# Optimization experiments

Measured on AMD Instinct MI355X. Metric: run time of the kernel, lower is better.

The kernel has to match this reference:

```python
import jax, jax.numpy as jnp
import numpy as np

N_LAYERS = 6
D_MODEL = 272          # num_variables
D_STATE = 64           # d_state
D_INNER = 2 * D_MODEL  # expand=2 -> 544
D_CONV = 4
DT_RANK = 17           # ceil(272/16)
N_SCORES = 4
B, L = 4, 2048


def setup_inputs():
    key = jax.random.key(0)
    ks = jax.random.split(key, 10)
    def rn(k, shape, s=0.02):
        return jax.random.normal(k, shape, dtype=jnp.float32) * s
    A_init = jnp.broadcast_to(jnp.arange(1, D_STATE + 1, dtype=jnp.float32), (N_LAYERS, D_INNER, D_STATE))
    return {
        "x": jax.random.normal(ks[0], (B, L, D_MODEL), dtype=jnp.float32),
        "ln_w": jnp.ones((N_LAYERS, D_MODEL), jnp.float32),
        "ln_b": jnp.zeros((N_LAYERS, D_MODEL), jnp.float32),
        "in_proj_w": rn(ks[1], (N_LAYERS, 2 * D_INNER, D_MODEL)),
        "conv_w": rn(ks[2], (N_LAYERS, D_INNER, D_CONV), 0.2),
        "conv_b": jnp.zeros((N_LAYERS, D_INNER), jnp.float32),
        "x_proj_w": rn(ks[3], (N_LAYERS, DT_RANK + 2 * D_STATE, D_INNER)),
        "dt_proj_w": rn(ks[4], (N_LAYERS, D_INNER, DT_RANK), 0.1),
        "dt_proj_b": rn(ks[5], (N_LAYERS, D_INNER), 0.5),
        "A_log": jnp.log(A_init),
        "Dskip": jnp.ones((N_LAYERS, D_INNER), jnp.float32),
        "out_proj_w": rn(ks[6], (N_LAYERS, D_MODEL, D_INNER)),
        "reg_w": rn(ks[7], (N_SCORES, D_MODEL)),
        "reg_b": jnp.zeros((N_SCORES,), jnp.float32),
    }


def _layernorm(x, w, b, eps=1e-5):
    mu = x.mean(-1, keepdims=True)
    var = ((x - mu) ** 2).mean(-1, keepdims=True)
    return (x - mu) * jax.lax.rsqrt(var + eps) * w + b


def _selective_scan(u, delta, A, Bm, C, Dd):
    # u, delta: (b,l,d); Bm, C: (b,l,n); A: (d,n); Dd: (d,)
    def step(h, inp):
        d_t, B_t, C_t, u_t = inp                           # (b,d),(b,n),(b,n),(b,d)
        dA = jnp.exp(d_t[:, :, None] * A)                  # (b,d,n)
        h = dA * h + (d_t * u_t)[:, :, None] * B_t[:, None, :]
        return h, jnp.einsum('bdn,bn->bd', h, C_t)
    h0 = jnp.zeros((u.shape[0], A.shape[0], A.shape[1]), u.dtype)
    xs = tuple(jnp.swapaxes(a, 0, 1) for a in (delta, Bm, C, u))  # time-major
    _, ys = jax.lax.scan(step, h0, xs)
    return jnp.swapaxes(ys, 0, 1) + u * Dd


def _mamba_block(x, ln_w, ln_b, Wi, cw, cb, Wx, Wdt, bdt, A_log, Dd, Wo):
    h = _layernorm(x, ln_w, ln_b)
    xi, z = jnp.split(h @ Wi.T, 2, axis=-1)                # (b,l,d_inner) each
    xp = jnp.pad(xi, ((0, 0), (D_CONV - 1, 0), (0, 0)))    # causal depthwise conv
    xc = sum(xp[:, k:k + xi.shape[1], :] * cw[:, k] for k in range(D_CONV)) + cb
    xc = jax.nn.silu(xc)
    dbl = xc @ Wx.T                                        # (b,l,dt_rank+2n)
    dt, Bm, C = jnp.split(dbl, [DT_RANK, DT_RANK + D_STATE], axis=-1)
    delta = jax.nn.softplus(dt @ Wdt.T + bdt)
    y = _selective_scan(xc, delta, -jnp.exp(A_log), Bm, C, Dd)
    y = y * jax.nn.silu(z)
    return x + y @ Wo.T                                    # residual


def reference(x, ln_w, ln_b, in_proj_w, conv_w, conv_b, x_proj_w, dt_proj_w, dt_proj_b, A_log, Dskip, out_proj_w, reg_w, reg_b):
    for i in range(N_LAYERS):
        x = _mamba_block(x, ln_w[i], ln_b[i], in_proj_w[i], conv_w[i], conv_b[i],
                         x_proj_w[i], dt_proj_w[i], dt_proj_b[i], A_log[i], Dskip[i], out_proj_w[i])
    feat = x.mean(axis=1)                                  # (b, d_model)
    scores = feat @ reg_w.T + reg_b                        # (b, n_scores)
    return (scores, feat)
```

## Files before the change

### kernel.cpp

```cpp
#include <hip/hip_runtime.h>
#include <hip/hip_bf16.h>
#include <math.h>

#define NL 6
#define DM 272
#define DS 64
#define DI 544
#define DTR 17
#define NSC 4
#define BB 4
#define LL 2048
#define MTOK (BB*LL)
#define TCH 128
#define CH  16
#define DQ  (DI/4)

typedef __attribute__((ext_vector_type(8))) short bf16x8;
typedef __attribute__((ext_vector_type(4))) float f32x4;

__device__ __forceinline__ float sigmoidf_(float x){ return 1.0f/(1.0f+__expf(-x)); }
__device__ __forceinline__ unsigned short f2bfu(float x){
    union { __hip_bfloat16 h; unsigned short u; } c; c.h = __float2bfloat16(x); return c.u;
}
__device__ __forceinline__ float bfu2f(unsigned short u){ return __uint_as_float(((unsigned)u)<<16); }
__device__ __forceinline__ float exp2x(float x){ float r; asm("v_exp_f32 %0, %1" : "=v"(r) : "v"(x)); return r; }

#define DPPADD(x, ctrl) x += __int_as_float(__builtin_amdgcn_update_dpp(0, __float_as_int(x), ctrl, 0xf, 0xf, true))
__device__ __forceinline__ float wsum64(float x){
    DPPADD(x, 0x111); DPPADD(x, 0x112); DPPADD(x, 0x114); DPPADD(x, 0x118);
    DPPADD(x, 0x142); DPPADD(x, 0x143);
    return x;
}

__global__ __launch_bounds__(256) void ln_kernel(const float* __restrict__ X,
                          const float* __restrict__ w,
                          const float* __restrict__ b,
                          unsigned short* __restrict__ Hb)
{
    int wave = threadIdx.x >> 6;
    int lane = threadIdx.x & 63;
    int tok = blockIdx.x*4 + wave;
    const float* xr = X + (size_t)tok*DM;
    float v[5];
    float s=0.f, ss=0.f;
    #pragma unroll
    for (int j=0;j<5;++j){
        int idx = lane + j*64;
        float x = (idx < DM) ? xr[idx] : 0.f;
        v[j]=x; s+=x; ss+=x*x;
    }
    #pragma unroll
    for (int off=1; off<64; off<<=1){ s += __shfl_xor(s,off); ss += __shfl_xor(ss,off); }
    float mu  = s * (1.0f/DM);
    float var = ss*(1.0f/DM) - mu*mu;
    float inv = 1.0f/sqrtf(var + 1e-5f);
    unsigned short* hr = Hb + (size_t)tok*DM;
    #pragma unroll
    for (int j=0;j<5;++j){
        int idx = lane + j*64;
        if (idx<DM) hr[idx] = f2bfu((v[j]-mu)*inv*w[idx] + b[idx]);
    }
}

template<bool RESID, bool OUTBF16>
__global__ __launch_bounds__(256) void gmfma(const unsigned short* __restrict__ A, int lda,
                     const unsigned short* __restrict__ W, int ldw,
                     void* __restrict__ Cv, int ldc,
                     const float* __restrict__ R, int ldr,
                     int N, int K)
{
    __shared__ unsigned short As[128*40];
    __shared__ unsigned short Bs[128*40];
    int bm = blockIdx.x*128, bn = blockIdx.y*128;
    int tid = threadIdx.x;
    int lane = tid & 63, wave = tid >> 6;
    int wm = wave >> 1, wn = wave & 1;
    f32x4 acc[4][4] = {};
    int r16 = lane & 15, kg = (lane >> 4) * 8;
    for (int k0=0; k0<K; k0+=32){
        #pragma unroll
        for (int it=0; it<2; ++it){
            int cid = tid + it*256;
            int row = cid >> 2, kq = (cid & 3)*8;
            int kk = k0 + kq;
            uint4 za = make_uint4(0,0,0,0);
            if (kk < K) za = *(const uint4*)(A + (size_t)(bm+row)*lda + kk);
            *(uint4*)&As[row*40 + kq] = za;
            uint4 zb = make_uint4(0,0,0,0);
            int wr = bn + row;
            if (wr < N && kk < K) zb = *(const uint4*)(W + (size_t)wr*ldw + kk);
            *(uint4*)&Bs[row*40 + kq] = zb;
        }
        __syncthreads();
        bf16x8 af[4], bfr[4];
        #pragma unroll
        for (int mi=0; mi<4; ++mi)
            af[mi] = *(bf16x8*)&As[(wm*64 + mi*16 + r16)*40 + kg];
        #pragma unroll
        for (int ni=0; ni<4; ++ni)
            bfr[ni] = *(bf16x8*)&Bs[(wn*64 + ni*16 + r16)*40 + kg];
        #pragma unroll
        for (int mi=0; mi<4; ++mi)
            #pragma unroll
            for (int ni=0; ni<4; ++ni)
                acc[mi][ni] = __builtin_amdgcn_mfma_f32_16x16x32_bf16(af[mi], bfr[ni], acc[mi][ni], 0, 0, 0);
        __syncthreads();
    }
    int rowt = (lane >> 4)*4, colt = lane & 15;
    #pragma unroll
    for (int mi=0; mi<4; ++mi){
        #pragma unroll
        for (int ni=0; ni<4; ++ni){
            int col = bn + wn*64 + ni*16 + colt;
            if (col < N){
                #pragma unroll
                for (int j=0; j<4; ++j){
                    int row = bm + wm*64 + mi*16 + rowt + j;
                    float v = acc[mi][ni][j];
                    if (RESID) v += R[(size_t)row*ldr + col];
                    if (OUTBF16)
                        ((unsigned short*)Cv)[(size_t)row*ldc + col] = f2bfu(v);
                    else
                        ((float*)Cv)[(size_t)row*ldc + col] = v;
                }
            }
        }
    }
}

__global__ __launch_bounds__(256) void conv_t2_kernel(const unsigned short* __restrict__ XZb,
                                 const float* __restrict__ cw,
                                 const float* __restrict__ cb,
                                 unsigned short* __restrict__ XCtb,
                                 unsigned short* __restrict__ Gtb,
                                 unsigned short* __restrict__ XCb)
{
    __shared__ float xi[67][69];
    __shared__ float zz[64][69];
    int bid = blockIdx.x;
    int b  = bid >> 8;
    int rem = bid & 255;
    int t0 = (rem >> 3)*64;
    int d0 = (rem & 7)*68;
    int tid = threadIdx.x;
    for (int li = tid; li < 67*17; li += 256){
        int row = li / 17, q = li - row*17;
        int tg = t0 - 3 + row;
        float4 v = make_float4(0.f,0.f,0.f,0.f);
        if (tg >= 0){
            ushort4 u4 = *(const ushort4*)(XZb + ((size_t)b*LL + tg)*(2*DI) + d0 + q*4);
            v.x = bfu2f(u4.x); v.y = bfu2f(u4.y); v.z = bfu2f(u4.z); v.w = bfu2f(u4.w);
        }
        xi[row][q*4+0]=v.x; xi[row][q*4+1]=v.y; xi[row][q*4+2]=v.z; xi[row][q*4+3]=v.w;
    }
    for (int li = tid; li < 64*17; li += 256){
        int row = li / 17, q = li - row*17;
        ushort4 u4 = *(const ushort4*)(XZb + ((size_t)b*LL + t0 + row)*(2*DI) + DI + d0 + q*4);
        zz[row][q*4+0]=bfu2f(u4.x); zz[row][q*4+1]=bfu2f(u4.y);
        zz[row][q*4+2]=bfu2f(u4.z); zz[row][q*4+3]=bfu2f(u4.w);
    }
    __syncthreads();
    int t = tid & 63;
    int dw = tid >> 6;
    float xcreg[17];
    #pragma unroll
    for (int i=0; i<17; ++i){
        int dl = dw + i*4;
        int d = d0 + dl;
        const float* cwd = cw + d*4;
        float acc = cb[d];
        #pragma unroll
        for (int k=0;k<4;++k) acc = fmaf(xi[t+k][dl], cwd[k], acc);
        float xc = acc * sigmoidf_(acc);
        float z  = zz[t][dl];
        size_t o = ((size_t)b*DI + d)*LL + t0 + t;
        XCtb[o] = f2bfu(xc);
        Gtb[o]  = f2bfu(z * sigmoidf_(z));
        xcreg[i] = xc;
    }
    __syncthreads();
    #pragma unroll
    for (int i=0; i<17; ++i) zz[t][dw + i*4] = xcreg[i];
    __syncthreads();
    for (int li = tid; li < 64*17; li += 256){
        int row = li / 17, q = li - row*17;
        ushort4 v;
        v.x = f2bfu(zz[row][q*4+0]); v.y = f2bfu(zz[row][q*4+1]);
        v.z = f2bfu(zz[row][q*4+2]); v.w = f2bfu(zz[row][q*4+3]);
        *(ushort4*)&XCb[((size_t)b*LL + t0 + row)*DI + d0 + q*4] = v;
    }
}

__global__ __launch_bounds__(256) void dt_t2_kernel(const float* __restrict__ DBLb,
                          const float* __restrict__ Wdt,
                          const float* __restrict__ bdt,
                          float* __restrict__ DELt)
{
    __shared__ float dtv[64*19];
    __shared__ float wl[68*17];
    int bid = blockIdx.x;
    int b  = bid >> 8;
    int rem = bid & 255;
    int t0 = (rem >> 3)*64;
    int d0 = (rem & 7)*68;
    int tid = threadIdx.x;
    for (int li = tid; li < 64*17; li += 256){
        int row = li / 17, col = li - row*17;
        dtv[row*19 + col] = DBLb[((size_t)b*LL + t0 + row)*145 + col];
    }
    for (int li = tid; li < 68*17; li += 256)
        wl[li] = Wdt[(size_t)d0*17 + li];
    __syncthreads();
    int t = tid & 63;
    #pragma unroll 1
    for (int dl = tid >> 6; dl < 68; dl += 4){
        float s = bdt[d0 + dl];
        #pragma unroll
        for (int r=0;r<DTR;++r) s = fmaf(dtv[t*19 + r], wl[dl*17 + r], s);
        float sp = (s > 20.f) ? s : log1pf(__expf(s));
        DELt[((size_t)b*DI + d0 + dl)*LL + t0 + t] = sp;
    }
}

__global__ __launch_bounds__(256) void scan_a(const float* __restrict__ DELt,
                       const unsigned short* __restrict__ XCtb,
                       const float* __restrict__ DBLb,
                       const float* __restrict__ A_log,
                       float* __restrict__ Q,
                       float* __restrict__ S)
{
    __shared__ float2 dlb[4][4][64];
    __shared__ float Bsh[64][68];
    int tid = threadIdx.x;
    int wave = tid >> 6, lane = tid & 63;
    float2 (*Db)[64] = dlb[wave];
    int wid = blockIdx.x*4 + wave;
    int dd = wid % DQ;
    int c  = (wid / DQ) % CH;
    int b  = wid / (DQ*CH);
    int d0 = dd, d1 = dd+DQ, d2 = dd+2*DQ, d3 = dd+3*DQ;
    const float L2E = 1.44269504f;
    float Av0 = -__expf(A_log[d0*DS + lane]) * L2E;
    float Av1 = -__expf(A_log[d1*DS + lane]) * L2E;
    float Av2 = -__expf(A_log[d2*DS + lane]) * L2E;
    float Av3 = -__expf(A_log[d3*DS + lane]) * L2E;
    float h0=0.f,h1=0.f,h2=0.f,h3=0.f, ds0=0.f,ds1=0.f,ds2=0.f,ds3=0.f;
    size_t rb0 = ((size_t)b*DI + d0)*LL + c*TCH;
    size_t rb1 = ((size_t)b*DI + d1)*LL + c*TCH;
    size_t rb2 = ((size_t)b*DI + d2)*LL + c*TCH;
    size_t rb3 = ((size_t)b*DI + d3)*LL + c*TCH;
    const float* pBB = DBLb + ((size_t)b*LL + (size_t)c*TCH)*145;
    float rg[16];
    #pragma unroll
    for (int k=0;k<16;++k){
        int li = tid + k*256;
        rg[k] = pBB[(size_t)(li>>6)*145 + 17 + (li&63)];
    }
    for (int blk=0; blk<TCH/64; ++blk){
        __syncthreads();
        #pragma unroll
        for (int k=0;k<16;++k){
            int li = tid + k*256;
            Bsh[li>>6][li&63] = rg[k];
        }
        __syncthreads();
        if (blk+1 < TCH/64){
            const float* nb = pBB + (size_t)(blk+1)*64*145;
            #pragma unroll
            for (int k=0;k<16;++k){
                int li = tid + k*256;
                rg[k] = nb[(size_t)(li>>6)*145 + 17 + (li&63)];
            }
        }
        size_t o0 = rb0 + blk*64 + lane, o1 = rb1 + blk*64 + lane;
        size_t o2 = rb2 + blk*64 + lane, o3 = rb3 + blk*64 + lane;
        float dl0 = DELt[o0], dl1 = DELt[o1], dl2 = DELt[o2], dl3 = DELt[o3];
        float du0 = dl0*bfu2f(XCtb[o0]), du1 = dl1*bfu2f(XCtb[o1]);
        float du2 = dl2*bfu2f(XCtb[o2]), du3 = dl3*bfu2f(XCtb[o3]);
        ds0 += dl0; ds1 += dl1; ds2 += dl2; ds3 += dl3;
        Db[0][lane] = make_float2(dl0, du0);
        Db[1][lane] = make_float2(dl1, du1);
        Db[2][lane] = make_float2(dl2, du2);
        Db[3][lane] = make_float2(dl3, du3);
        #pragma unroll 1
        for (int g=0; g<8; ++g){
            const float2* q0 = &Db[0][g*8];
            const float2* q1 = &Db[1][g*8];
            const float2* q2 = &Db[2][g*8];
            const float2* q3 = &Db[3][g*8];
            #pragma unroll
            for (int i=0; i<8; ++i){
                float Bv = Bsh[g*8+i][lane];
                float2 a0=q0[i], a1=q1[i], a2=q2[i], a3=q3[i];
                h0 = fmaf(exp2x(a0.x*Av0), h0, a0.y*Bv);
                h1 = fmaf(exp2x(a1.x*Av1), h1, a1.y*Bv);
                h2 = fmaf(exp2x(a2.x*Av2), h2, a2.y*Bv);
                h3 = fmaf(exp2x(a3.x*Av3), h3, a3.y*Bv);
            }
        }
    }
    size_t q0i = ((size_t)b*DI + d0)*CH + c, q1i = ((size_t)b*DI + d1)*CH + c;
    size_t q2i = ((size_t)b*DI + d2)*CH + c, q3i = ((size_t)b*DI + d3)*CH + c;
    Q[q0i*64 + lane] = h0; Q[q1i*64 + lane] = h1;
    Q[q2i*64 + lane] = h2; Q[q3i*64 + lane] = h3;
    float s0 = wsum64(ds0), s1 = wsum64(ds1), s2 = wsum64(ds2), s3 = wsum64(ds3);
    if (lane == 63){ S[q0i]=s0; S[q1i]=s1; S[q2i]=s2; S[q3i]=s3; }
}

__global__ __launch_bounds__(256) void scan_c(const float* __restrict__ DELt,
                       const unsigned short* __restrict__ XCtb,
                       const unsigned short* __restrict__ Gtb,
                       const float* __restrict__ DBLb,
                       const float* __restrict__ A_log,
                       const float* __restrict__ Dskip,
                       const float* __restrict__ Q,
                       const float* __restrict__ S,
                       unsigned short* __restrict__ Yb)
{
    __shared__ float P[4][2][4][76];
    __shared__ float Ypark[4][2][4];
    __shared__ float2 dlb[4][2][64];
    __shared__ unsigned short Yst[64][12];
    int tid = threadIdx.x;
    int wave = tid >> 6, lane = tid & 63;
    float (*Pr0)[76] = P[wave][0];
    float (*Pr1)[76] = P[wave][1];
    float* Yp0 = Ypark[wave][0];
    float* Yp1 = Ypark[wave][1];
    float2* Db0 = dlb[wave][0];
    float2* Db1 = dlb[wave][1];
    int wid = blockIdx.x*4 + wave;
    int dd = wid % (DI/2);
    int c  = (wid / (DI/2)) % CH;
    int b  = wid / ((DI/2)*CH);
    int d0 = dd, d1 = dd + DI/2;
    int wid0 = blockIdx.x*4;
    int dd0b = wid0 % (DI/2);
    int cB = (wid0 / (DI/2)) % CH;
    int bB = wid0 / ((DI/2)*CH);
    const float L2E = 1.44269504f;
    float Av0 = -__expf(A_log[d0*DS + lane]) * L2E;
    float Av1 = -__expf(A_log[d1*DS + lane]) * L2E;
    float Dd0 = Dskip[d0], Dd1 = Dskip[d1];
    size_t q0 = ((size_t)b*DI + d0)*CH, q1 = ((size_t)b*DI + d1)*CH;
    float h0=0.f, h1=0.f;
    for (int j=0; j<c; ++j){
        h0 = fmaf(exp2x(Av0*S[q0+j]), h0, Q[(q0+j)*64 + lane]);
        h1 = fmaf(exp2x(Av1*S[q1+j]), h1, Q[(q1+j)*64 + lane]);
    }
    size_t rb0 = ((size_t)b*DI + d0)*LL + c*TCH;
    size_t rb1 = ((size_t)b*DI + d1)*LL + c*TCH;
    const float* pB = DBLb + ((size_t)b*LL + c*TCH)*145;
    int fr = lane >> 4, fq = (lane & 15)*4;
    for (int blk=0; blk<TCH/64; ++blk){
        size_t o0 = rb0 + blk*64 + lane, o1 = rb1 + blk*64 + lane;
        float dl0 = DELt[o0], dl1 = DELt[o1];
        float ul0 = bfu2f(XCtb[o0]), ul1 = bfu2f(XCtb[o1]);
        float gl0 = bfu2f(Gtb[o0]),  gl1 = bfu2f(Gtb[o1]);
        Db0[lane] = make_float2(dl0, dl0*ul0);
        Db1[lane] = make_float2(dl1, dl1*ul1);
        float y0=0.f, y1=0.f;
        const float* p = pB + (size_t)blk*64*145;
        #pragma unroll 1
        for (int f=0; f<16; ++f){
            const float2* db0 = &Db0[f*4];
            const float2* db1 = &Db1[f*4];
            #pragma unroll
            for (int i=0; i<4; ++i){
                float Bv = p[17+lane];
                float Cv = p[81+lane];
                float2 a0 = db0[i], a1 = db1[i];
                h0 = fmaf(exp2x(a0.x*Av0), h0, a0.y*Bv);
                h1 = fmaf(exp2x(a1.x*Av1), h1, a1.y*Bv);
                Pr0[i][lane] = h0*Cv;
                Pr1[i][lane] = h1*Cv;
                p += 145;
            }
            float4 xa0 = *(const float4*)&Pr0[fr][fq];
            float s0 = (xa0.x+xa0.y)+(xa0.z+xa0.w);
            DPPADD(s0,0x111); DPPADD(s0,0x112); DPPADD(s0,0x114); DPPADD(s0,0x118);
            float4 xa1 = *(const float4*)&Pr1[fr][fq];
            float s1 = (xa1.x+xa1.y)+(xa1.z+xa1.w);
            DPPADD(s1,0x111); DPPADD(s1,0x112); DPPADD(s1,0x114); DPPADD(s1,0x118);
            if ((lane & 15) == 15){ Yp0[fr] = s0; Yp1[fr] = s1; }
            float g0 = Yp0[lane & 3];
            float g1 = Yp1[lane & 3];
            if ((lane >> 2) == f){ y0 = g0; y1 = g1; }
        }
        Yst[lane][wave]     = f2bfu((y0 + ul0*Dd0)*gl0);
        Yst[lane][4 + wave] = f2bfu((y1 + ul1*Dd1)*gl1);
        __syncthreads();
        if (tid < 128){
            int row = tid & 63, grp = tid >> 6;
            ushort4 v = *(const ushort4*)&Yst[row][grp*4];
            size_t trow = (size_t)bB*LL + (size_t)cB*TCH + blk*64 + row;
            *(ushort4*)&Yb[trow*DI + dd0b + grp*(DI/2)] = v;
        }
        __syncthreads();
    }
}

__global__ __launch_bounds__(256) void wconv_kernel(const float* __restrict__ src,
                            unsigned short* __restrict__ dst,
                            int total, int kin, int kout)
{
    int idx = blockIdx.x*256 + threadIdx.x;
    if (idx >= total) return;
    int r = idx / kout, c = idx - r*kout;
    float v = (c < kin) ? src[(size_t)r*kin + c] : 0.f;
    dst[idx] = f2bfu(v);
}

__global__ __launch_bounds__(256) void head1_kernel(const float* __restrict__ X,
                             float* __restrict__ Pt)
{
    int b = blockIdx.x >> 6, c = blockIdx.x & 63;
    int tid = threadIdx.x;
    for (int dm = tid; dm < DM; dm += 256){
        float s = 0.f;
        const float* base = X + ((size_t)b*LL + c*32)*DM + dm;
        #pragma unroll 8
        for (int tt=0; tt<32; ++tt) s += base[(size_t)tt*DM];
        Pt[(size_t)(b*64 + c)*DM + dm] = s;
    }
}

__global__ __launch_bounds__(256) void head2_kernel(const float* __restrict__ Pt,
                             const float* __restrict__ reg_w,
                             const float* __restrict__ reg_b,
                             float* __restrict__ out)
{
    __shared__ float feat[DM];
    int b = blockIdx.x, tid = threadIdx.x;
    for (int dm = tid; dm < DM; dm += 256){
        float s = 0.f;
        for (int c=0; c<64; ++c) s += Pt[(size_t)(b*64 + c)*DM + dm];
        float f = s * (1.0f/LL);
        feat[dm] = f;
        out[16 + b*DM + dm] = f;
    }
    __syncthreads();
    if (tid < NSC){
        float s = reg_b[tid];
        const float* wr = reg_w + tid*DM;
        for (int k=0;k<DM;++k) s = fmaf(feat[k], wr[k], s);
        out[b*NSC + tid] = s;
    }
}

extern "C" void kernel_launch(void* const* d_in, const int* in_sizes, int n_in,
                              void* d_out, int out_size, void* d_ws, size_t ws_size,
                              hipStream_t stream)
{
    const float* x_in  = (const float*)d_in[0];
    const float* ln_w  = (const float*)d_in[1];
    const float* ln_b  = (const float*)d_in[2];
    const float* Wi    = (const float*)d_in[3];
    const float* cw    = (const float*)d_in[4];
    const float* cb    = (const float*)d_in[5];
    const float* Wx    = (const float*)d_in[6];
    const float* Wdt   = (const float*)d_in[7];
    const float* bdt   = (const float*)d_in[8];
    const float* A_log = (const float*)d_in[9];
    const float* Dd    = (const float*)d_in[10];
    const float* Wo    = (const float*)d_in[11];
    const float* regw  = (const float*)d_in[12];
    const float* regb  = (const float*)d_in[13];
    float* out = (float*)d_out;

    char* base = (char*)d_ws;
    auto carve = [&](size_t bytes) -> char* {
        char* p = base; base += (bytes + 255) & ~(size_t)255; return p;
    };
    unsigned short* XZb  = (unsigned short*)carve((size_t)MTOK*1088*2);
    unsigned short* XCtb = (unsigned short*)carve((size_t)MTOK*544*2);
    unsigned short* Gtb  = (unsigned short*)carve((size_t)MTOK*544*2);
    float*          DELt = (float*)carve((size_t)MTOK*544*4);
    float*          DBLb = (float*)carve((size_t)MTOK*145*4);
    float*          Xb   = (float*)carve((size_t)MTOK*272*4);
    unsigned short* Yb   = (unsigned short*)carve((size_t)MTOK*544*2);
    char*           SCR  = carve((size_t)MTOK*272*4);
    float*          Sbuf = (float*)carve((size_t)BB*DI*CH*4);
    unsigned short* WiB  = (unsigned short*)carve((size_t)NL*1088*DM*2);
    unsigned short* WxB  = (unsigned short*)carve((size_t)NL*145*DI*2);
    unsigned short* WoB  = (unsigned short*)carve((size_t)NL*272*DI*2);

    unsigned short* Hb  = (unsigned short*)SCR;
    unsigned short* XCb = (unsigned short*)SCR;
    float*          Q   = (float*)SCR;
    float*          Pt  = (float*)SCR;

    (void)hipMemcpyAsync(Xb, x_in, sizeof(float)*(size_t)MTOK*DM, hipMemcpyDeviceToDevice, stream);

    wconv_kernel<<<(NL*1088*DM + 255)/256, 256, 0, stream>>>(Wi, WiB, NL*1088*DM, DM, DM);
    wconv_kernel<<<(NL*145*DI + 255)/256, 256, 0, stream>>>(Wx, WxB, NL*145*DI, DI, DI);
    wconv_kernel<<<(NL*272*DI + 255)/256, 256, 0, stream>>>(Wo, WoB, NL*272*DI, DI, DI);

    for (int l=0; l<NL; ++l){
        ln_kernel<<<MTOK/4, 256, 0, stream>>>(Xb, ln_w + l*DM, ln_b + l*DM, Hb);
        gmfma<false,true><<<dim3(MTOK/128, (2*DI+127)/128), 256, 0, stream>>>(
            Hb, DM, WiB + (size_t)l*2*DI*DM, DM, XZb, 2*DI, nullptr, 0, 2*DI, DM);
        conv_t2_kernel<<<BB*256, 256, 0, stream>>>(XZb, cw + l*DI*4, cb + l*DI, XCtb, Gtb, XCb);
        gmfma<false,false><<<dim3(MTOK/128, 2), 256, 0, stream>>>(
            XCb, DI, WxB + (size_t)l*145*DI, DI, DBLb, 145, nullptr, 0, 145, DI);
        dt_t2_kernel<<<BB*256, 256, 0, stream>>>(DBLb, Wdt + (size_t)l*DI*DTR, bdt + l*DI, DELt);
        scan_a<<<(BB*CH*DQ)/4, 256, 0, stream>>>(DELt, XCtb, DBLb,
                                                 A_log + (size_t)l*DI*DS, Q, Sbuf);
        scan_c<<<(BB*CH*(DI/2))/4, 256, 0, stream>>>(DELt, XCtb, Gtb, DBLb,
                                                     A_log + (size_t)l*DI*DS, Dd + l*DI, Q, Sbuf, Yb);
        gmfma<true,false><<<dim3(MTOK/128, 3), 256, 0, stream>>>(
            Yb, DI, WoB + (size_t)l*DM*DI, DI, Xb, DM, Xb, DM, DM, DI);
    }
    head1_kernel<<<BB*64, 256, 0, stream>>>(Xb, Pt);
    head2_kernel<<<BB, 256, 0, stream>>>(Pt, regw, regb, out);
}
```

Before: 1.587 ms.

## Fuse dt projection and softplus into scan kernels, pack u and gate

Removes the separate dt_t2 kernel and its fp32 delta buffer: both scan passes now recompute delta from the 17 dt-rank values in DBL with a fast exp2/log2 softplus. The conv kernel writes u and the silu gate as one packed 32-bit word instead of two separate bf16 arrays. scan_a also drops its shared-memory staging of B and reads B straight from global memory. This saves one launch and a large amount of global memory traffic, at the cost of doing the dt projection twice and making uncoalesced strided loads of the DBL rows.

```diff
diff --git a/kernel.cpp b/kernel.cpp
--- a/kernel.cpp
+++ b/kernel.cpp
@@ -24,6 +24,11 @@
 }
 __device__ __forceinline__ float bfu2f(unsigned short u){ return __uint_as_float(((unsigned)u)<<16); }
 __device__ __forceinline__ float exp2x(float x){ float r; asm("v_exp_f32 %0, %1" : "=v"(r) : "v"(x)); return r; }
+__device__ __forceinline__ float log2x(float x){ float r; asm("v_log_f32 %0, %1" : "=v"(r) : "v"(x)); return r; }
+__device__ __forceinline__ float softplus_(float s){
+    float sp = 0.6931471806f * log2x(1.0f + exp2x(s * 1.44269504f));
+    return (s > 20.f) ? s : sp;
+}
 
 #define DPPADD(x, ctrl) x += __int_as_float(__builtin_amdgcn_update_dpp(0, __float_as_int(x), ctrl, 0xf, 0xf, true))
 __device__ __forceinline__ float wsum64(float x){
@@ -131,8 +136,7 @@
 __global__ __launch_bounds__(256) void conv_t2_kernel(const unsigned short* __restrict__ XZb,
                                  const float* __restrict__ cw,
                                  const float* __restrict__ cb,
-                                 unsigned short* __restrict__ XCtb,
-                                 unsigned short* __restrict__ Gtb,
+                                 unsigned int* __restrict__ UGt,
                                  unsigned short* __restrict__ XCb)
 {
     __shared__ float xi[67][69];
@@ -174,8 +178,8 @@
         float xc = acc * sigmoidf_(acc);
         float z  = zz[t][dl];
         size_t o = ((size_t)b*DI + d)*LL + t0 + t;
-        XCtb[o] = f2bfu(xc);
-        Gtb[o]  = f2bfu(z * sigmoidf_(z));
+        float g = z * sigmoidf_(z);
+        UGt[o] = (unsigned int)f2bfu(xc) | ((unsigned int)f2bfu(g) << 16);
         xcreg[i] = xc;
     }
     __syncthreads();
@@ -191,46 +195,15 @@
     }
 }
 
-__global__ __launch_bounds__(256) void dt_t2_kernel(const float* __restrict__ DBLb,
-                          const float* __restrict__ Wdt,
-                          const float* __restrict__ bdt,
-                          float* __restrict__ DELt)
-{
-    __shared__ float dtv[64*19];
-    __shared__ float wl[68*17];
-    int bid = blockIdx.x;
-    int b  = bid >> 8;
-    int rem = bid & 255;
-    int t0 = (rem >> 3)*64;
-    int d0 = (rem & 7)*68;
-    int tid = threadIdx.x;
-    for (int li = tid; li < 64*17; li += 256){
-        int row = li / 17, col = li - row*17;
-        dtv[row*19 + col] = DBLb[((size_t)b*LL + t0 + row)*145 + col];
-    }
-    for (int li = tid; li < 68*17; li += 256)
-        wl[li] = Wdt[(size_t)d0*17 + li];
-    __syncthreads();
-    int t = tid & 63;
-    #pragma unroll 1
-    for (int dl = tid >> 6; dl < 68; dl += 4){
-        float s = bdt[d0 + dl];
-        #pragma unroll
-        for (int r=0;r<DTR;++r) s = fmaf(dtv[t*19 + r], wl[dl*17 + r], s);
-        float sp = (s > 20.f) ? s : log1pf(__expf(s));
-        DELt[((size_t)b*DI + d0 + dl)*LL + t0 + t] = sp;
-    }
-}
-
-__global__ __launch_bounds__(256) void scan_a(const float* __restrict__ DELt,
-                       const unsigned short* __restrict__ XCtb,
+__global__ __launch_bounds__(256) void scan_a(const unsigned int* __restrict__ UGt,
                        const float* __restrict__ DBLb,
+                       const float* __restrict__ Wdt,
+                       const float* __restrict__ bdt,
                        const float* __restrict__ A_log,
                        float* __restrict__ Q,
                        float* __restrict__ S)
 {
     __shared__ float2 dlb[4][4][64];
-    __shared__ float Bsh[64][68];
     int tid = threadIdx.x;
     int wave = tid >> 6, lane = tid & 63;
     float2 (*Db)[64] = dlb[wave];
@@ -244,44 +217,40 @@
     float Av1 = -__expf(A_log[d1*DS + lane]) * L2E;
     float Av2 = -__expf(A_log[d2*DS + lane]) * L2E;
     float Av3 = -__expf(A_log[d3*DS + lane]) * L2E;
+    float bd0 = bdt[d0], bd1 = bdt[d1], bd2 = bdt[d2], bd3 = bdt[d3];
     float h0=0.f,h1=0.f,h2=0.f,h3=0.f, ds0=0.f,ds1=0.f,ds2=0.f,ds3=0.f;
     size_t rb0 = ((size_t)b*DI + d0)*LL + c*TCH;
     size_t rb1 = ((size_t)b*DI + d1)*LL + c*TCH;
     size_t rb2 = ((size_t)b*DI + d2)*LL + c*TCH;
     size_t rb3 = ((size_t)b*DI + d3)*LL + c*TCH;
-    const float* pBB = DBLb + ((size_t)b*LL + (size_t)c*TCH)*145;
-    float rg[16];
-    #pragma unroll
-    for (int k=0;k<16;++k){
-        int li = tid + k*256;
-        rg[k] = pBB[(size_t)(li>>6)*145 + 17 + (li&63)];
-    }
+    const float* pB = DBLb + ((size_t)b*LL + (size_t)c*TCH)*145;
     for (int blk=0; blk<TCH/64; ++blk){
-        __syncthreads();
-        #pragma unroll
-        for (int k=0;k<16;++k){
-            int li = tid + k*256;
-            Bsh[li>>6][li&63] = rg[k];
-        }
-        __syncthreads();
-        if (blk+1 < TCH/64){
-            const float* nb = pBB + (size_t)(blk+1)*64*145;
-            #pragma unroll
-            for (int k=0;k<16;++k){
-                int li = tid + k*256;
-                rg[k] = nb[(size_t)(li>>6)*145 + 17 + (li&63)];
-            }
-        }
+        const float* dp = pB + (size_t)(blk*64 + lane)*145;
+        float dv[17];
+        #pragma unroll
+        for (int r=0;r<17;++r) dv[r] = dp[r];
+        float s0=bd0, s1=bd1, s2=bd2, s3=bd3;
+        #pragma unroll
+        for (int r=0;r<17;++r){
+            s0 = fmaf(dv[r], Wdt[d0*DTR+r], s0);
+            s1 = fmaf(dv[r], Wdt[d1*DTR+r], s1);
+            s2 = fmaf(dv[r], Wdt[d2*DTR+r], s2);
+            s3 = fmaf(dv[r], Wdt[d3*DTR+r], s3);
+        }
+        float dl0 = softplus_(s0), dl1 = softplus_(s1);
+        float dl2 = softplus_(s2), dl3 = softplus_(s3);
         size_t o0 = rb0 + blk*64 + lane, o1 = rb1 + blk*64 + lane;
         size_t o2 = rb2 + blk*64 + lane, o3 = rb3 + blk*64 + lane;
-        float dl0 = DELt[o0], dl1 = DELt[o1], dl2 = DELt[o2], dl3 = DELt[o3];
-        float du0 = dl0*bfu2f(XCtb[o0]), du1 = dl1*bfu2f(XCtb[o1]);
-        float du2 = dl2*bfu2f(XCtb[o2]), du3 = dl3*bfu2f(XCtb[o3]);
+        float du0 = dl0*bfu2f((unsigned short)UGt[o0]);
+        float du1 = dl1*bfu2f((unsigned short)UGt[o1]);
+        float du2 = dl2*bfu2f((unsigned short)UGt[o2]);
+        float du3 = dl3*bfu2f((unsigned short)UGt[o3]);
         ds0 += dl0; ds1 += dl1; ds2 += dl2; ds3 += dl3;
         Db[0][lane] = make_float2(dl0, du0);
         Db[1][lane] = make_float2(dl1, du1);
         Db[2][lane] = make_float2(dl2, du2);
         Db[3][lane] = make_float2(dl3, du3);
+        const float* p = pB + (size_t)blk*64*145;
         #pragma unroll 1
         for (int g=0; g<8; ++g){
             const float2* q0 = &Db[0][g*8];
@@ -290,12 +259,13 @@
             const float2* q3 = &Db[3][g*8];
             #pragma unroll
             for (int i=0; i<8; ++i){
-                float Bv = Bsh[g*8+i][lane];
+                float Bv = p[17+lane];
                 float2 a0=q0[i], a1=q1[i], a2=q2[i], a3=q3[i];
                 h0 = fmaf(exp2x(a0.x*Av0), h0, a0.y*Bv);
                 h1 = fmaf(exp2x(a1.x*Av1), h1, a1.y*Bv);
                 h2 = fmaf(exp2x(a2.x*Av2), h2, a2.y*Bv);
                 h3 = fmaf(exp2x(a3.x*Av3), h3, a3.y*Bv);
+                p += 145;
             }
         }
     }
@@ -303,14 +273,14 @@
     size_t q2i = ((size_t)b*DI + d2)*CH + c, q3i = ((size_t)b*DI + d3)*CH + c;
     Q[q0i*64 + lane] = h0; Q[q1i*64 + lane] = h1;
     Q[q2i*64 + lane] = h2; Q[q3i*64 + lane] = h3;
-    float s0 = wsum64(ds0), s1 = wsum64(ds1), s2 = wsum64(ds2), s3 = wsum64(ds3);
-    if (lane == 63){ S[q0i]=s0; S[q1i]=s1; S[q2i]=s2; S[q3i]=s3; }
-}
-
-__global__ __launch_bounds__(256) void scan_c(const float* __restrict__ DELt,
-                       const unsigned short* __restrict__ XCtb,
-                       const unsigned short* __restrict__ Gtb,
+    float s0w = wsum64(ds0), s1w = wsum64(ds1), s2w = wsum64(ds2), s3w = wsum64(ds3);
+    if (lane == 63){ S[q0i]=s0w; S[q1i]=s1w; S[q2i]=s2w; S[q3i]=s3w; }
+}
+
+__global__ __launch_bounds__(256) void scan_c(const unsigned int* __restrict__ UGt,
                        const float* __restrict__ DBLb,
+                       const float* __restrict__ Wdt,
+                       const float* __restrict__ bdt,
                        const float* __restrict__ A_log,
                        const float* __restrict__ Dskip,
                        const float* __restrict__ Q,
@@ -342,6 +312,7 @@
     float Av0 = -__expf(A_log[d0*DS + lane]) * L2E;
     float Av1 = -__expf(A_log[d1*DS + lane]) * L2E;
     float Dd0 = Dskip[d0], Dd1 = Dskip[d1];
+    float bd0 = bdt[d0], bd1 = bdt[d1];
     size_t q0 = ((size_t)b*DI + d0)*CH, q1 = ((size_t)b*DI + d1)*CH;
     float h0=0.f, h1=0.f;
     for (int j=0; j<c; ++j){
@@ -353,10 +324,21 @@
     const float* pB = DBLb + ((size_t)b*LL + c*TCH)*145;
     int fr = lane >> 4, fq = (lane & 15)*4;
     for (int blk=0; blk<TCH/64; ++blk){
+        const float* dp = pB + (size_t)(blk*64 + lane)*145;
+        float dv[17];
+        #pragma unroll
+        for (int r=0;r<17;++r) dv[r] = dp[r];
+        float s0=bd0, s1=bd1;
+        #pragma unroll
+        for (int r=0;r<17;++r){
+            s0 = fmaf(dv[r], Wdt[d0*DTR+r], s0);
+            s1 = fmaf(dv[r], Wdt[d1*DTR+r], s1);
+        }
+        float dl0 = softplus_(s0), dl1 = softplus_(s1);
         size_t o0 = rb0 + blk*64 + lane, o1 = rb1 + blk*64 + lane;
-        float dl0 = DELt[o0], dl1 = DELt[o1];
-        float ul0 = bfu2f(XCtb[o0]), ul1 = bfu2f(XCtb[o1]);
-        float gl0 = bfu2f(Gtb[o0]),  gl1 = bfu2f(Gtb[o1]);
+        unsigned int ug0 = UGt[o0], ug1 = UGt[o1];
+        float ul0 = bfu2f((unsigned short)ug0), ul1 = bfu2f((unsigned short)ug1);
+        float gl0 = bfu2f((unsigned short)(ug0 >> 16)), gl1 = bfu2f((unsigned short)(ug1 >> 16));
         Db0[lane] = make_float2(dl0, dl0*ul0);
         Db1[lane] = make_float2(dl1, dl1*ul1);
         float y0=0.f, y1=0.f;
@@ -377,12 +359,12 @@
                 p += 145;
             }
             float4 xa0 = *(const float4*)&Pr0[fr][fq];
-            float s0 = (xa0.x+xa0.y)+(xa0.z+xa0.w);
-            DPPADD(s0,0x111); DPPADD(s0,0x112); DPPADD(s0,0x114); DPPADD(s0,0x118);
+            float s0f = (xa0.x+xa0.y)+(xa0.z+xa0.w);
+            DPPADD(s0f,0x111); DPPADD(s0f,0x112); DPPADD(s0f,0x114); DPPADD(s0f,0x118);
             float4 xa1 = *(const float4*)&Pr1[fr][fq];
-            float s1 = (xa1.x+xa1.y)+(xa1.z+xa1.w);
-            DPPADD(s1,0x111); DPPADD(s1,0x112); DPPADD(s1,0x114); DPPADD(s1,0x118);
-            if ((lane & 15) == 15){ Yp0[fr] = s0; Yp1[fr] = s1; }
+            float s1f = (xa1.x+xa1.y)+(xa1.z+xa1.w);
+            DPPADD(s1f,0x111); DPPADD(s1f,0x112); DPPADD(s1f,0x114); DPPADD(s1f,0x118);
+            if ((lane & 15) == 15){ Yp0[fr] = s0f; Yp1[fr] = s1f; }
             float g0 = Yp0[lane & 3];
             float g1 = Yp1[lane & 3];
             if ((lane >> 2) == f){ y0 = g0; y1 = g1; }
@@ -473,9 +455,7 @@
         char* p = base; base += (bytes + 255) & ~(size_t)255; return p;
     };
     unsigned short* XZb  = (unsigned short*)carve((size_t)MTOK*1088*2);
-    unsigned short* XCtb = (unsigned short*)carve((size_t)MTOK*544*2);
-    unsigned short* Gtb  = (unsigned short*)carve((size_t)MTOK*544*2);
-    float*          DELt = (float*)carve((size_t)MTOK*544*4);
+    unsigned int*   UGt  = (unsigned int*)carve((size_t)MTOK*544*4);
     float*          DBLb = (float*)carve((size_t)MTOK*145*4);
     float*          Xb   = (float*)carve((size_t)MTOK*272*4);
     unsigned short* Yb   = (unsigned short*)carve((size_t)MTOK*544*2);
@@ -500,13 +480,12 @@
         ln_kernel<<<MTOK/4, 256, 0, stream>>>(Xb, ln_w + l*DM, ln_b + l*DM, Hb);
         gmfma<false,true><<<dim3(MTOK/128, (2*DI+127)/128), 256, 0, stream>>>(
             Hb, DM, WiB + (size_t)l*2*DI*DM, DM, XZb, 2*DI, nullptr, 0, 2*DI, DM);
-        conv_t2_kernel<<<BB*256, 256, 0, stream>>>(XZb, cw + l*DI*4, cb + l*DI, XCtb, Gtb, XCb);
+        conv_t2_kernel<<<BB*256, 256, 0, stream>>>(XZb, cw + l*DI*4, cb + l*DI, UGt, XCb);
         gmfma<false,false><<<dim3(MTOK/128, 2), 256, 0, stream>>>(
             XCb, DI, WxB + (size_t)l*145*DI, DI, DBLb, 145, nullptr, 0, 145, DI);
-        dt_t2_kernel<<<BB*256, 256, 0, stream>>>(DBLb, Wdt + (size_t)l*DI*DTR, bdt + l*DI, DELt);
-        scan_a<<<(BB*CH*DQ)/4, 256, 0, stream>>>(DELt, XCtb, DBLb,
+        scan_a<<<(BB*CH*DQ)/4, 256, 0, stream>>>(UGt, DBLb, Wdt + (size_t)l*DI*DTR, bdt + l*DI,
                                                  A_log + (size_t)l*DI*DS, Q, Sbuf);
-        scan_c<<<(BB*CH*(DI/2))/4, 256, 0, stream>>>(DELt, XCtb, Gtb, DBLb,
+        scan_c<<<(BB*CH*(DI/2))/4, 256, 0, stream>>>(UGt, DBLb, Wdt + (size_t)l*DI*DTR, bdt + l*DI,
                                                      A_log + (size_t)l*DI*DS, Dd + l*DI, Q, Sbuf, Yb);
         gmfma<true,false><<<dim3(MTOK/128, 3), 256, 0, stream>>>(
             Yb, DI, WoB + (size_t)l*DM*DI, DI, Xb, DM, Xb, DM, DM, DI);
```

Result: no change. 1.562 ms (-1.6%).
